# Optimization experiments

Measured on AMD Instinct MI355X. Metric: run time of the kernel, lower is better.

## Reference

```python
import jax, jax.numpy as jnp
import numpy as np

D_MODEL = 1024
NUM_HEADS = 16
D_K = D_MODEL // NUM_HEADS
D_FF = 4096
EPS = 1e-5


def _layer_norm(x, g, b):
    mu = jnp.mean(x, axis=-1, keepdims=True)
    var = jnp.mean(jnp.square(x - mu), axis=-1, keepdims=True)
    return (x - mu) * jax.lax.rsqrt(var + EPS) * g + b


def setup_inputs() -> dict:
    key = jax.random.key(0)
    ks = jax.random.split(key, 16)
    s = 0.02
    inp = {
        "x": jax.random.normal(ks[0], (2, 2048, D_MODEL), dtype=jnp.float32),
        # attention projections, torch Linear convention: W [out, in]
        "wq": jax.random.normal(ks[1], (D_MODEL, D_MODEL), dtype=jnp.float32) * s,
        "bq": jnp.zeros((D_MODEL,), jnp.float32),
        "wk": jax.random.normal(ks[2], (D_MODEL, D_MODEL), dtype=jnp.float32) * s,
        "bk": jnp.zeros((D_MODEL,), jnp.float32),
        "wv": jax.random.normal(ks[3], (D_MODEL, D_MODEL), dtype=jnp.float32) * s,
        "bv": jnp.zeros((D_MODEL,), jnp.float32),
        "wo": jax.random.normal(ks[4], (D_MODEL, D_MODEL), dtype=jnp.float32) * s,
        "bo": jnp.zeros((D_MODEL,), jnp.float32),
        "ln1_g": jnp.ones((D_MODEL,), jnp.float32),
        "ln1_b": jnp.zeros((D_MODEL,), jnp.float32),
        "w1": jax.random.normal(ks[5], (D_FF, D_MODEL), dtype=jnp.float32) * s,
        "b1": jnp.zeros((D_FF,), jnp.float32),
        "w2": jax.random.normal(ks[6], (D_MODEL, D_FF), dtype=jnp.float32) * s,
        "b2": jnp.zeros((D_MODEL,), jnp.float32),
        "ln2_g": jnp.ones((D_MODEL,), jnp.float32),
        "ln2_b": jnp.zeros((D_MODEL,), jnp.float32),
    }
    return inp


def reference(x, wq, bq, wk, bk, wv, bv, wo, bo, ln1_g, ln1_b,
              w1, b1, w2, b2, ln2_g, ln2_b):
    B, S, D = x.shape
    H, Dk = NUM_HEADS, D_K
    # projections -> [B, H, S, Dk]
    q = (x @ wq.T + bq).reshape(B, S, H, Dk).transpose(0, 2, 1, 3)
    k = (x @ wk.T + bk).reshape(B, S, H, Dk).transpose(0, 2, 1, 3)
    v = (x @ wv.T + bv).reshape(B, S, H, Dk).transpose(0, 2, 1, 3)
    # explicit [B,H,S,S] scores (faithful to source, memory-bound)
    scores = jnp.einsum("bhqd,bhkd->bhqk", q, k) / jnp.sqrt(jnp.float32(Dk))
    attn = jax.nn.softmax(scores, axis=-1)
    ctx = jnp.einsum("bhqk,bhkd->bhqd", attn, v)
    ctx = ctx.transpose(0, 2, 1, 3).reshape(B, S, D)
    attn_out = _layer_norm(ctx @ wo.T + bo + x, ln1_g, ln1_b)
    # feed-forward (post-LN residual), GELU (erf, torch default)
    h = jax.nn.gelu(attn_out @ w1.T + b1, approximate=False)
    ff = h @ w2.T + b2
    return _layer_norm(ff + attn_out, ln2_g, ln2_b)
```

## Files before the change

### kernel.cpp

```cpp
#include <hip/hip_runtime.h>
#include <math.h>

#define DM   1024
#define SL   2048
#define NB   2
#define NH   16
#define DKH  64
#define DFF  4096
#define NTOK 4096

typedef unsigned short u16;
typedef unsigned int u32;
typedef __attribute__((ext_vector_type(8))) short bf16x8;
typedef __attribute__((ext_vector_type(4))) float f32x4;
typedef __attribute__((ext_vector_type(16))) float f32x16;

typedef __attribute__((address_space(1))) void gvoid;
typedef __attribute__((address_space(3))) void lvoid;

#define QSCALE 0.18033688011112042f

__device__ __forceinline__ u16 f2bf(float f) {
  union { float f; unsigned u; } v; v.f = f;
  unsigned r = (v.u + 0x7fffu + ((v.u >> 16) & 1u)) >> 16;
  return (u16)r;
}
__device__ __forceinline__ float bf2f(u16 h) {
  union { unsigned u; float f; } v; v.u = ((unsigned)h) << 16; return v.f;
}
__device__ __forceinline__ void gld16(const u16* g, u16* l) {
  __builtin_amdgcn_global_load_lds((gvoid*)g, (lvoid*)l, 16, 0, 0);
}

__global__ __launch_bounds__(256)
void cvt_all(const float* __restrict__ x,  const float* __restrict__ wq,
             const float* __restrict__ wk, const float* __restrict__ wv,
             const float* __restrict__ wo, const float* __restrict__ w1,
             const float* __restrict__ w2,
             u16* __restrict__ xb, u16* __restrict__ wqb, u16* __restrict__ wkb,
             u16* __restrict__ wvb, u16* __restrict__ wob, u16* __restrict__ w1b,
             u16* __restrict__ w2b) {
  const int total = 4194304;
  for (int i = blockIdx.x * blockDim.x + threadIdx.x; i < total;
       i += gridDim.x * blockDim.x) {
    const float* src; u16* dst; int off;
    if      (i < 1048576) { src = x;  dst = xb;  off = i; }
    else if (i < 1310720) { src = wq; dst = wqb; off = i - 1048576; }
    else if (i < 1572864) { src = wk; dst = wkb; off = i - 1310720; }
    else if (i < 1835008) { src = wv; dst = wvb; off = i - 1572864; }
    else if (i < 2097152) { src = wo; dst = wob; off = i - 1835008; }
    else if (i < 3145728) { src = w1; dst = w1b; off = i - 2097152; }
    else                  { src = w2; dst = w2b; off = i - 3145728; }
    float4 v = ((const float4*)src)[off];
    ushort4 o = { f2bf(v.x), f2bf(v.y), f2bf(v.z), f2bf(v.w) };
    ((ushort4*)dst)[off] = o;
  }
}

#define BM 128
#define BN 128
#define BK 64

template <int EPI>
__global__ __launch_bounds__(256, 2)
void gemm_bt(const u16* __restrict__ A, const u16* __restrict__ W,
             const float* __restrict__ bias, const float* __restrict__ residf,
             const u16* __restrict__ residb, void* __restrict__ out,
             int M, int N, int K) {
  __shared__ u16 smem[2][2][BM * BK];
  const int tid = threadIdx.x;
  const int lane = tid & 63;
  const int wid  = tid >> 6;
  const int r16  = lane & 15;
  const int hi   = lane >> 4;
  const int wm = wid >> 1, wn = wid & 1;
  const int bm = blockIdx.x * BM;
  const int bn = blockIdx.y * BN;

  const int srow  = tid >> 3;
  const int sslot = (tid & 7) ^ (srow & 7);
  const size_t aoff = (size_t)(bm + srow) * K + sslot * 8;
  const size_t boff = (size_t)(bn + srow) * K + sslot * 8;

  f32x4 acc[4][4] = {};
  const int nk = K / BK;
  int cur = 0;

  auto STAGE = [&](int buf, int kt) {
    const u16* ga = A + aoff + kt * BK;
    const u16* gb = W + boff + kt * BK;
    u16* la = &smem[buf][0][wid * 512];
    u16* lb = &smem[buf][1][wid * 512];
#pragma unroll
    for (int i = 0; i < 4; ++i) {
      gld16(ga + (size_t)i * 32 * K, la + i * 2048);
      gld16(gb + (size_t)i * 32 * K, lb + i * 2048);
    }
  };

  STAGE(0, 0);
  __syncthreads();

  for (int kt = 0; kt < nk; ++kt) {
    if (kt + 1 < nk) STAGE(cur ^ 1, kt + 1);
    const u16* la = &smem[cur][0][0];
    const u16* lb = &smem[cur][1][0];
#pragma unroll
    for (int kk = 0; kk < 2; ++kk) {
      const int swz = ((kk * 4 + hi) ^ (r16 & 7)) * 8;
      bf16x8 af[4], bfr[4];
#pragma unroll
      for (int i = 0; i < 4; ++i)
        af[i] = *(const bf16x8*)&la[(wm * 64 + i * 16 + r16) * 64 + swz];
#pragma unroll
      for (int j = 0; j < 4; ++j)
        bfr[j] = *(const bf16x8*)&lb[(wn * 64 + j * 16 + r16) * 64 + swz];
      __builtin_amdgcn_s_setprio(1);
#pragma unroll
      for (int i = 0; i < 4; ++i)
#pragma unroll
        for (int j = 0; j < 4; ++j)
          acc[i][j] = __builtin_amdgcn_mfma_f32_16x16x32_bf16(af[i], bfr[j],
                                                              acc[i][j], 0, 0, 0);
      __builtin_amdgcn_s_setprio(0);
    }
    __syncthreads();
    cur ^= 1;
  }

#pragma unroll
  for (int i = 0; i < 4; ++i) {
#pragma unroll
    for (int j = 0; j < 4; ++j) {
      const int c  = bn + wn * 64 + j * 16 + r16;
      const int r0 = bm + wm * 64 + i * 16 + hi * 4;
      const float bv = bias[c];
#pragma unroll
      for (int rr = 0; rr < 4; ++rr) {
        const int r = r0 + rr;
        float v = acc[i][j][rr] + bv;
        if (EPI == 3) {
          ((float*)out)[(size_t)r * N + c] = v + residf[(size_t)r * N + c];
        } else if (EPI == 4) {
          const float gl = 0.5f * v * (1.0f + erff(v * 0.7071067811865475f));
          ((u16*)out)[(size_t)r * N + c] = f2bf(gl);
        } else {
          ((float*)out)[(size_t)r * N + c] = v + bf2f(residb[(size_t)r * N + c]);
        }
      }
    }
  }
}

__global__ __launch_bounds__(256, 2)
void gemm_qkv(const u16* __restrict__ A, const u16* __restrict__ wq,
              const u16* __restrict__ wk, const u16* __restrict__ wv,
              const float* __restrict__ bq, const float* __restrict__ bk,
              const float* __restrict__ bv,
              u16* __restrict__ qo, u16* __restrict__ ko, u16* __restrict__ vo) {
  __shared__ u16 smem[2][2][BM * BK];
  const int tid = threadIdx.x;
  const int lane = tid & 63;
  const int wid  = tid >> 6;
  const int r16  = lane & 15;
  const int hi   = lane >> 4;
  const int wm = wid >> 1, wn = wid & 1;
  const int bm = blockIdx.x * BM;
  const int sel = blockIdx.y >> 3;
  const int bn  = (blockIdx.y & 7) * BN;
  const u16* W = sel == 0 ? wq : sel == 1 ? wk : wv;
  const float* bias = sel == 0 ? bq : sel == 1 ? bk : bv;
  const int K = DM, N = DM;

  const int srow  = tid >> 3;
  const int sslot = (tid & 7) ^ (srow & 7);
  const size_t aoff = (size_t)(bm + srow) * K + sslot * 8;
  const size_t boff = (size_t)(bn + srow) * K + sslot * 8;

  f32x4 acc[4][4] = {};
  int cur = 0;

  auto STAGE = [&](int buf, int kt) {
    const u16* ga = A + aoff + kt * BK;
    const u16* gb = W + boff + kt * BK;
    u16* la = &smem[buf][0][wid * 512];
    u16* lb = &smem[buf][1][wid * 512];
#pragma unroll
    for (int i = 0; i < 4; ++i) {
      gld16(ga + (size_t)i * 32 * K, la + i * 2048);
      gld16(gb + (size_t)i * 32 * K, lb + i * 2048);
    }
  };

  STAGE(0, 0);
  __syncthreads();

  for (int kt = 0; kt < 16; ++kt) {
    if (kt + 1 < 16) STAGE(cur ^ 1, kt + 1);
    const u16* la = &smem[cur][0][0];
    const u16* lb = &smem[cur][1][0];
#pragma unroll
    for (int kk = 0; kk < 2; ++kk) {
      const int swz = ((kk * 4 + hi) ^ (r16 & 7)) * 8;
      bf16x8 af[4], bfr[4];
#pragma unroll
      for (int i = 0; i < 4; ++i)
        af[i] = *(const bf16x8*)&la[(wm * 64 + i * 16 + r16) * 64 + swz];
#pragma unroll
      for (int j = 0; j < 4; ++j)
        bfr[j] = *(const bf16x8*)&lb[(wn * 64 + j * 16 + r16) * 64 + swz];
      __builtin_amdgcn_s_setprio(1);
#pragma unroll
      for (int i = 0; i < 4; ++i)
#pragma unroll
        for (int j = 0; j < 4; ++j)
          acc[i][j] = __builtin_amdgcn_mfma_f32_16x16x32_bf16(af[i], bfr[j],
                                                              acc[i][j], 0, 0, 0);
      __builtin_amdgcn_s_setprio(0);
    }
    __syncthreads();
    cur ^= 1;
  }

#pragma unroll
  for (int i = 0; i < 4; ++i) {
#pragma unroll
    for (int j = 0; j < 4; ++j) {
      const int c  = bn + wn * 64 + j * 16 + r16;
      const int r0 = bm + wm * 64 + i * 16 + hi * 4;
      const float bvv = bias[c];
#pragma unroll
      for (int rr = 0; rr < 4; ++rr) {
        const int r = r0 + rr;
        const float v = acc[i][j][rr] + bvv;
        if (sel == 0) {
          qo[(size_t)r * N + c] = f2bf(v * QSCALE);
        } else if (sel == 1) {
          ko[(size_t)r * N + c] = f2bf(v);
        } else {
          const int b = r >> 11, s = r & 2047;
          const int hh = c >> 6, dk = c & 63;
          vo[((size_t)((b * NH + hh) * DKH + dk)) * SL + s] = f2bf(v);
        }
      }
    }
  }
}

__global__ __launch_bounds__(256, 2)
void attn(const u16* __restrict__ q, const u16* __restrict__ k,
          const u16* __restrict__ vt, u16* __restrict__ ctx) {
  __shared__ u16 kl[2][64 * 64];
  __shared__ u16 vl[2][64 * 64];

  const int tid = threadIdx.x;
  const int lane = tid & 63, wid = tid >> 6;
  const int l31 = lane & 31, h = lane >> 5;
  const int rs = l31 & 7;
  const int bh = blockIdx.x, b = bh >> 4, hh = bh & 15;
  const int qg = blockIdx.y * 128 + wid * 32 + l31;

  bf16x8 qf[4];
#pragma unroll
  for (int kq = 0; kq < 4; ++kq)
    qf[kq] = *(const bf16x8*)(q + (size_t)(b * SL + qg) * DM + hh * DKH +
                              kq * 16 + h * 8);

  f32x16 o0 = {}, o1 = {};
  float mrun = -1e30f, lrun = 0.f;

  const int srow  = tid >> 3;
  const int sslot = (tid & 7) ^ (srow & 7);

  auto STAGE = [&](int buf, int t) {
    const u16* gk = k + (size_t)(b * SL + t * 64 + srow) * DM + hh * DKH + sslot * 8;
    const u16* gv = vt + (size_t)(bh * DKH + srow) * SL + t * 64 + sslot * 8;
    u16* lk = &kl[buf][wid * 512];
    u16* lv = &vl[buf][wid * 512];
#pragma unroll
    for (int i = 0; i < 2; ++i) {
      gld16(gk + (size_t)i * 32 * DM, lk + i * 2048);
      gld16(gv + (size_t)i * 32 * SL, lv + i * 2048);
    }
  };

  auto TILE = [&](int buf) {
    const u16* lk = kl[buf];
    const u16* lv = vl[buf];
    f32x16 s0 = {}, s1 = {};
    __builtin_amdgcn_s_setprio(1);
#pragma unroll
    for (int kq = 0; kq < 4; ++kq) {
      const int ls = 2 * kq + h;
      bf16x8 k0 = *(const bf16x8*)&lk[l31 * 64 + ((ls ^ rs) * 8)];
      bf16x8 k1 = *(const bf16x8*)&lk[(l31 + 32) * 64 + ((ls ^ rs) * 8)];
      s0 = __builtin_amdgcn_mfma_f32_32x32x16_bf16(k0, qf[kq], s0, 0, 0, 0);
      s1 = __builtin_amdgcn_mfma_f32_32x32x16_bf16(k1, qf[kq], s1, 0, 0, 0);
    }
    __builtin_amdgcn_s_setprio(0);

    float mx = fmaxf(s0[0], s0[1]);
#pragma unroll
    for (int r = 2; r < 16; ++r) mx = fmaxf(mx, s0[r]);
#pragma unroll
    for (int r = 0; r < 16; ++r) mx = fmaxf(mx, s1[r]);
    {
      float ta = mx, tb = mx;
      asm volatile("v_permlane32_swap_b32 %0, %1" : "+v"(ta), "+v"(tb));
      mx = fmaxf(ta, tb);
    }
    if (!__all(mx <= mrun + 11.0f)) {
      const float mn = fmaxf(mrun, mx);
      const float al = __builtin_amdgcn_exp2f(mrun - mn);
      mrun = mn;
      lrun *= al;
      o0 *= al; o1 *= al;
    }
    float lsum = 0.f;
#pragma unroll
    for (int r = 0; r < 16; ++r) {
      s0[r] = __builtin_amdgcn_exp2f(s0[r] - mrun); lsum += s0[r];
    }
#pragma unroll
    for (int r = 0; r < 16; ++r) {
      s1[r] = __builtin_amdgcn_exp2f(s1[r] - mrun); lsum += s1[r];
    }
    lrun += lsum;

    u32 A[16];
#pragma unroll
    for (int r = 0; r < 8; ++r)
      asm("v_cvt_pk_bf16_f32 %0, %1, %2"
          : "=v"(A[r]) : "v"(s0[2 * r]), "v"(s0[2 * r + 1]));
#pragma unroll
    for (int r = 0; r < 8; ++r)
      asm("v_cvt_pk_bf16_f32 %0, %1, %2"
          : "=v"(A[8 + r]) : "v"(s1[2 * r]), "v"(s1[2 * r + 1]));
#pragma unroll
    for (int g = 0; g < 4; ++g) {
      asm volatile("v_permlane32_swap_b32 %0, %1" : "+v"(A[4 * g + 0]), "+v"(A[4 * g + 2]));
      asm volatile("v_permlane32_swap_b32 %0, %1" : "+v"(A[4 * g + 1]), "+v"(A[4 * g + 3]));
    }

    __builtin_amdgcn_s_setprio(1);
#pragma unroll
    for (int ks = 0; ks < 4; ++ks) {
      union { u32 u[4]; bf16x8 hv; } pb;
      pb.u[0] = A[4 * ks + 0]; pb.u[1] = A[4 * ks + 1];
      pb.u[2] = A[4 * ks + 2]; pb.u[3] = A[4 * ks + 3];
      const int ls = 2 * ks + h;
      bf16x8 v0 = *(const bf16x8*)&lv[l31 * 64 + ((ls ^ rs) * 8)];
      bf16x8 v1 = *(const bf16x8*)&lv[(l31 + 32) * 64 + ((ls ^ rs) * 8)];
      o0 = __builtin_amdgcn_mfma_f32_32x32x16_bf16(v0, pb.hv, o0, 0, 0, 0);
      o1 = __builtin_amdgcn_mfma_f32_32x32x16_bf16(v1, pb.hv, o1, 0, 0, 0);
    }
    __builtin_amdgcn_s_setprio(0);
  };

  STAGE(0, 0);
  __syncthreads();
  int cur = 0;
  for (int t = 0; t < SL / 64; ++t) {
    if (t + 1 < SL / 64) STAGE(cur ^ 1, t + 1);
    TILE(cur);
    __syncthreads();
    cur ^= 1;
  }

  float ta = lrun, tb = lrun;
  asm volatile("v_permlane32_swap_b32 %0, %1" : "+v"(ta), "+v"(tb));
  const float rl = 1.f / (ta + tb);
  const size_t obase = (size_t)(b * SL + qg) * DM + hh * DKH;
#pragma unroll
  for (int df = 0; df < 2; ++df) {
#pragma unroll
    for (int r2 = 0; r2 < 4; ++r2) {
      const int dk0 = 8 * r2 + 4 * h + 32 * df;
      ushort4 st;
      if (df == 0) {
        st.x = f2bf(o0[4 * r2 + 0] * rl); st.y = f2bf(o0[4 * r2 + 1] * rl);
        st.z = f2bf(o0[4 * r2 + 2] * rl); st.w = f2bf(o0[4 * r2 + 3] * rl);
      } else {
        st.x = f2bf(o1[4 * r2 + 0] * rl); st.y = f2bf(o1[4 * r2 + 1] * rl);
        st.z = f2bf(o1[4 * r2 + 2] * rl); st.w = f2bf(o1[4 * r2 + 3] * rl);
      }
      *(ushort4*)(ctx + obase + dk0) = st;
    }
  }
}

__global__ __launch_bounds__(256)
void ln_k(const float* __restrict__ in, const float* __restrict__ g,
          const float* __restrict__ be, float* __restrict__ outf,
          u16* __restrict__ outb) {
  const int row = blockIdx.x;
  const int tid = threadIdx.x;
  const float4 x4 = ((const float4*)(in + (size_t)row * DM))[tid];
  float s  = x4.x + x4.y + x4.z + x4.w;
  float s2 = x4.x * x4.x + x4.y * x4.y + x4.z * x4.z + x4.w * x4.w;
#pragma unroll
  for (int d = 1; d < 64; d <<= 1) {
    s  += __shfl_xor(s, d);
    s2 += __shfl_xor(s2, d);
  }
  __shared__ float ps[8];
  const int wid = tid >> 6, lane = tid & 63;
  if (lane == 0) { ps[wid] = s; ps[wid + 4] = s2; }
  __syncthreads();
  const float S  = ps[0] + ps[1] + ps[2] + ps[3];
  const float S2 = ps[4] + ps[5] + ps[6] + ps[7];
  const float mu = S * (1.f / DM);
  const float var = S2 * (1.f / DM) - mu * mu;
  const float rstd = 1.f / sqrtf(var + 1e-5f);
  const float4 gv = ((const float4*)g)[tid];
  const float4 bv = ((const float4*)be)[tid];
  float4 o;
  o.x = (x4.x - mu) * rstd * gv.x + bv.x;
  o.y = (x4.y - mu) * rstd * gv.y + bv.y;
  o.z = (x4.z - mu) * rstd * gv.z + bv.z;
  o.w = (x4.w - mu) * rstd * gv.w + bv.w;
  if (outf) ((float4*)(outf + (size_t)row * DM))[tid] = o;
  if (outb) {
    ushort4 ob = { f2bf(o.x), f2bf(o.y), f2bf(o.z), f2bf(o.w) };
    ((ushort4*)(outb + (size_t)row * DM))[tid] = ob;
  }
}

extern "C" void kernel_launch(void* const* d_in, const int* in_sizes, int n_in,
                              void* d_out, int out_size, void* d_ws, size_t ws_size,
                              hipStream_t stream) {
  const float* x   = (const float*)d_in[0];
  const float* wq  = (const float*)d_in[1];
  const float* bq  = (const float*)d_in[2];
  const float* wk  = (const float*)d_in[3];
  const float* bk  = (const float*)d_in[4];
  const float* wv  = (const float*)d_in[5];
  const float* bv  = (const float*)d_in[6];
  const float* wo  = (const float*)d_in[7];
  const float* bo  = (const float*)d_in[8];
  const float* g1  = (const float*)d_in[9];
  const float* be1 = (const float*)d_in[10];
  const float* w1  = (const float*)d_in[11];
  const float* b1  = (const float*)d_in[12];
  const float* w2  = (const float*)d_in[13];
  const float* b2  = (const float*)d_in[14];
  const float* g2  = (const float*)d_in[15];
  const float* be2 = (const float*)d_in[16];

  if (ws_size < ((size_t)80 << 20)) return;

  char* ws = (char*)d_ws;
  u16*  xb   = (u16*)(ws);
  u16*  wqb  = (u16*)(ws + ((size_t)8  << 20));
  u16*  wkb  = (u16*)(ws + ((size_t)10 << 20));
  u16*  wvb  = (u16*)(ws + ((size_t)12 << 20));
  u16*  wob  = (u16*)(ws + ((size_t)14 << 20));
  u16*  w1b  = (u16*)(ws + ((size_t)16 << 20));
  u16*  w2b  = (u16*)(ws + ((size_t)24 << 20));
  u16*  qbuf = (u16*)(ws + ((size_t)32 << 20));
  u16*  kbuf = (u16*)(ws + ((size_t)40 << 20));
  u16*  vtb  = (u16*)(ws + ((size_t)48 << 20));
  u16*  ctx  = (u16*)(ws + ((size_t)56 << 20));
  float* ores = (float*)(ws + ((size_t)64 << 20));
  u16*  aob  = xb;
  u16*  hb   = qbuf;
  float* ff  = ores;

  float* out = (float*)d_out;
  dim3 blk(256);

  cvt_all<<<2048, blk, 0, stream>>>(x, wq, wk, wv, wo, w1, w2,
                                    xb, wqb, wkb, wvb, wob, w1b, w2b);
  gemm_qkv<<<dim3(32, 24), blk, 0, stream>>>(xb, wqb, wkb, wvb, bq, bk, bv,
                                             qbuf, kbuf, vtb);
  attn<<<dim3(32, 16), blk, 0, stream>>>(qbuf, kbuf, vtb, ctx);
  gemm_bt<3><<<dim3(32, 8), blk, 0, stream>>>(ctx, wob, bo, x, nullptr, ores, NTOK, DM, DM);
  ln_k<<<4096, blk, 0, stream>>>(ores, g1, be1, nullptr, aob);
  gemm_bt<4><<<dim3(32, 32), blk, 0, stream>>>(aob, w1b, b1, nullptr, nullptr, hb, NTOK, DFF, DM);
  gemm_bt<5><<<dim3(32, 8), blk, 0, stream>>>(hb, w2b, b2, nullptr, aob, ff, NTOK, DM, DFF);
  ln_k<<<4096, blk, 0, stream>>>(ff, g2, be2, out, nullptr);
}
```

Measured before the change: 235.0 us.

## Use 256x256-tile 8-wave GEMM with phased pipelining for QKV and FFN1

Adds a new gemm256 kernel with 256x256 output tiles, 512 threads (8 waves), half-tile staged double buffering, and interleaved LDS loads, MFMA bursts and barriers. It also remaps block IDs to group tiles for L2 locality. It replaces the 128x128 QKV GEMM and the GELU FFN1 GEMM, aiming to raise per-block data reuse and hide global-load latency. The cost is many more registers per thread (32 accumulator vectors), fewer blocks (192/256 on a large-CU device), and a more fragile hand-tuned sync schedule.

```diff
diff --git a/kernel.cpp b/kernel.cpp
--- a/kernel.cpp
+++ b/kernel.cpp
@@ -57,6 +57,146 @@
   }
 }
 
+template <int MODE>
+__global__ __launch_bounds__(512, 2)
+void gemm256(const u16* __restrict__ A, const u16* __restrict__ Wq,
+             const u16* __restrict__ Wk, const u16* __restrict__ Wv,
+             const float* __restrict__ Bq, const float* __restrict__ Bk,
+             const float* __restrict__ Bv,
+             u16* __restrict__ qo, u16* __restrict__ ko, u16* __restrict__ vo,
+             int K) {
+  __shared__ u16 lds[2][2][2][128 * 64];
+
+  const int tid  = threadIdx.x;
+  const int lane = tid & 63;
+  const int wid  = tid >> 6;
+  const int r16  = lane & 15;
+  const int hi   = lane >> 4;
+  const int wr   = wid >> 2;
+  const int wc   = wid & 3;
+  const int nkt  = K >> 6;
+
+  const int lid = blockIdx.y * 16 + blockIdx.x;
+  const int nwg = (MODE == 0) ? 192 : 256;
+  const int cpx = nwg >> 3;
+  const int l2  = (lid & 7) * cpx + (lid >> 3);
+  const int bx2 = l2 & 15, by2 = l2 >> 4;
+
+  const int bm  = bx2 * 256;
+  int sel = 0, bnl;
+  const u16* W; const float* bias;
+  if (MODE == 0) {
+    sel = by2 >> 2;  bnl = (by2 & 3) * 256;
+    W = sel == 0 ? Wq : sel == 1 ? Wk : Wv;
+    bias = sel == 0 ? Bq : sel == 1 ? Bk : Bv;
+  } else {
+    bnl = by2 * 256; W = Wq; bias = Bq;
+  }
+
+  const int strow = tid >> 3;
+  const int stslt = tid & 7;
+  const int ssrc  = stslt ^ (strow & 7);
+
+  auto STAGEH = [&](int kt, int op, int hf) {
+    const u16* src = (op == 0) ? A : W;
+    const int  gb  = (op == 0) ? bm : bnl;
+    const u16* g = src + (size_t)(gb + hf * 128 + strow) * K + kt * 64 + ssrc * 8;
+    u16* d = &lds[kt & 1][op][hf][tid * 8];
+    gld16(g, d);
+    gld16(g + (size_t)64 * K, d + 4096);
+  };
+
+  f32x4 acc[8][4] = {};
+
+  STAGEH(0, 1, 0); STAGEH(0, 1, 1); STAGEH(0, 0, 0); STAGEH(0, 0, 1);
+  STAGEH(1, 1, 0); STAGEH(1, 1, 1);
+  asm volatile("s_waitcnt vmcnt(4)" ::: "memory");
+  __builtin_amdgcn_s_barrier();
+
+#define GPHASE(PH, SKT, SOP, SHF, VMTAIL)                                     \
+  {                                                                           \
+    bf16x8 af[2][2];                                                          \
+    _Pragma("unroll")                                                         \
+    for (int mm = 0; mm < 2; ++mm)                                            \
+      _Pragma("unroll")                                                       \
+      for (int kk = 0; kk < 2; ++kk) {                                        \
+        const int row = ((PH) * 2 + mm) * 16 + r16;                           \
+        af[mm][kk] = *(const bf16x8*)&la[row * 64 +                           \
+                        (((kk * 4 + hi) ^ (r16 & 7)) * 8)];                   \
+      }                                                                       \
+    if ((PH) == 0) {                                                          \
+      _Pragma("unroll")                                                       \
+      for (int n = 0; n < 4; ++n)                                             \
+        _Pragma("unroll")                                                     \
+        for (int kk = 0; kk < 2; ++kk) {                                      \
+          const int row = brow0 + n * 16 + r16;                               \
+          bfr[n][kk] = *(const bf16x8*)&lbh[row * 64 +                        \
+                          (((kk * 4 + hi) ^ (r16 & 7)) * 8)];                 \
+        }                                                                     \
+    }                                                                         \
+    if ((SKT) < nkt) STAGEH((SKT), (SOP), (SHF));                             \
+    __builtin_amdgcn_s_barrier();                                             \
+    asm volatile("s_waitcnt lgkmcnt(0)" ::: "memory");                        \
+    __builtin_amdgcn_sched_barrier(0);                                        \
+    __builtin_amdgcn_s_setprio(1);                                            \
+    _Pragma("unroll")                                                         \
+    for (int mm = 0; mm < 2; ++mm)                                            \
+      _Pragma("unroll")                                                       \
+      for (int n = 0; n < 4; ++n)                                             \
+        _Pragma("unroll")                                                     \
+        for (int kk = 0; kk < 2; ++kk)                                        \
+          acc[(PH) * 2 + mm][n] = __builtin_amdgcn_mfma_f32_16x16x32_bf16(    \
+              af[mm][kk], bfr[n][kk], acc[(PH) * 2 + mm][n], 0, 0, 0);        \
+    __builtin_amdgcn_s_setprio(0);                                            \
+    if ((VMTAIL) == 1) {                                                      \
+      if (T < nkt - 2) { asm volatile("s_waitcnt vmcnt(4)" ::: "memory"); }   \
+      else             { asm volatile("s_waitcnt vmcnt(0)" ::: "memory"); }   \
+    }                                                                         \
+    __builtin_amdgcn_s_barrier();                                             \
+  }
+
+  for (int T = 0; T < nkt; ++T) {
+    const u16* la  = lds[T & 1][0][wr];
+    const u16* lbh = lds[T & 1][1][wc >> 1];
+    const int brow0 = (wc & 1) * 64;
+    bf16x8 bfr[4][2];
+    GPHASE(0, T + 1, 0, 0, 0)
+    GPHASE(1, T + 1, 0, 1, 0)
+    GPHASE(2, T + 2, 1, 0, 0)
+    GPHASE(3, T + 2, 1, 1, 1)
+  }
+#undef GPHASE
+
+#pragma unroll
+  for (int m = 0; m < 8; ++m) {
+#pragma unroll
+    for (int n = 0; n < 4; ++n) {
+      const int cg  = bnl + wc * 64 + n * 16 + r16;
+      const int rg0 = bm + wr * 128 + m * 16 + hi * 4;
+      const float bv = bias[cg];
+#pragma unroll
+      for (int rr = 0; rr < 4; ++rr) {
+        const int rg = rg0 + rr;
+        const float v = acc[m][n][rr] + bv;
+        if (MODE == 0) {
+          if (sel == 0) {
+            qo[(size_t)rg * DM + cg] = f2bf(v * QSCALE);
+          } else if (sel == 1) {
+            ko[(size_t)rg * DM + cg] = f2bf(v);
+          } else {
+            const int b = rg >> 11, s = rg & 2047;
+            const int hh = cg >> 6, dk = cg & 63;
+            vo[((size_t)((b * NH + hh) * DKH + dk)) * SL + s] = f2bf(v);
+          }
+        } else {
+          const float gl = 0.5f * v * (1.0f + erff(v * 0.7071067811865475f));
+          qo[(size_t)rg * DFF + cg] = f2bf(gl);
+        }
+      }
+    }
+  }
+}
+
 #define BM 128
 #define BN 128
 #define BK 64
@@ -141,106 +281,8 @@
         float v = acc[i][j][rr] + bv;
         if (EPI == 3) {
           ((float*)out)[(size_t)r * N + c] = v + residf[(size_t)r * N + c];
-        } else if (EPI == 4) {
-          const float gl = 0.5f * v * (1.0f + erff(v * 0.7071067811865475f));
-          ((u16*)out)[(size_t)r * N + c] = f2bf(gl);
         } else {
           ((float*)out)[(size_t)r * N + c] = v + bf2f(residb[(size_t)r * N + c]);
-        }
-      }
-    }
-  }
-}
-
-__global__ __launch_bounds__(256, 2)
-void gemm_qkv(const u16* __restrict__ A, const u16* __restrict__ wq,
-              const u16* __restrict__ wk, const u16* __restrict__ wv,
-              const float* __restrict__ bq, const float* __restrict__ bk,
-              const float* __restrict__ bv,
-              u16* __restrict__ qo, u16* __restrict__ ko, u16* __restrict__ vo) {
-  __shared__ u16 smem[2][2][BM * BK];
-  const int tid = threadIdx.x;
-  const int lane = tid & 63;
-  const int wid  = tid >> 6;
-  const int r16  = lane & 15;
-  const int hi   = lane >> 4;
-  const int wm = wid >> 1, wn = wid & 1;
-  const int bm = blockIdx.x * BM;
-  const int sel = blockIdx.y >> 3;
-  const int bn  = (blockIdx.y & 7) * BN;
-  const u16* W = sel == 0 ? wq : sel == 1 ? wk : wv;
-  const float* bias = sel == 0 ? bq : sel == 1 ? bk : bv;
-  const int K = DM, N = DM;
-
-  const int srow  = tid >> 3;
-  const int sslot = (tid & 7) ^ (srow & 7);
-  const size_t aoff = (size_t)(bm + srow) * K + sslot * 8;
-  const size_t boff = (size_t)(bn + srow) * K + sslot * 8;
-
-  f32x4 acc[4][4] = {};
-  int cur = 0;
-
-  auto STAGE = [&](int buf, int kt) {
-    const u16* ga = A + aoff + kt * BK;
-    const u16* gb = W + boff + kt * BK;
-    u16* la = &smem[buf][0][wid * 512];
-    u16* lb = &smem[buf][1][wid * 512];
-#pragma unroll
-    for (int i = 0; i < 4; ++i) {
-      gld16(ga + (size_t)i * 32 * K, la + i * 2048);
-      gld16(gb + (size_t)i * 32 * K, lb + i * 2048);
-    }
-  };
-
-  STAGE(0, 0);
-  __syncthreads();
-
-  for (int kt = 0; kt < 16; ++kt) {
-    if (kt + 1 < 16) STAGE(cur ^ 1, kt + 1);
-    const u16* la = &smem[cur][0][0];
-    const u16* lb = &smem[cur][1][0];
-#pragma unroll
-    for (int kk = 0; kk < 2; ++kk) {
-      const int swz = ((kk * 4 + hi) ^ (r16 & 7)) * 8;
-      bf16x8 af[4], bfr[4];
-#pragma unroll
-      for (int i = 0; i < 4; ++i)
-        af[i] = *(const bf16x8*)&la[(wm * 64 + i * 16 + r16) * 64 + swz];
-#pragma unroll
-      for (int j = 0; j < 4; ++j)
-        bfr[j] = *(const bf16x8*)&lb[(wn * 64 + j * 16 + r16) * 64 + swz];
-      __builtin_amdgcn_s_setprio(1);
-#pragma unroll
-      for (int i = 0; i < 4; ++i)
-#pragma unroll
-        for (int j = 0; j < 4; ++j)
-          acc[i][j] = __builtin_amdgcn_mfma_f32_16x16x32_bf16(af[i], bfr[j],
-                                                              acc[i][j], 0, 0, 0);
-      __builtin_amdgcn_s_setprio(0);
-    }
-    __syncthreads();
-    cur ^= 1;
-  }
-
-#pragma unroll
-  for (int i = 0; i < 4; ++i) {
-#pragma unroll
-    for (int j = 0; j < 4; ++j) {
-      const int c  = bn + wn * 64 + j * 16 + r16;
-      const int r0 = bm + wm * 64 + i * 16 + hi * 4;
-      const float bvv = bias[c];
-#pragma unroll
-      for (int rr = 0; rr < 4; ++rr) {
-        const int r = r0 + rr;
-        const float v = acc[i][j][rr] + bvv;
-        if (sel == 0) {
-          qo[(size_t)r * N + c] = f2bf(v * QSCALE);
-        } else if (sel == 1) {
-          ko[(size_t)r * N + c] = f2bf(v);
-        } else {
-          const int b = r >> 11, s = r & 2047;
-          const int hh = c >> 6, dk = c & 63;
-          vo[((size_t)((b * NH + hh) * DKH + dk)) * SL + s] = f2bf(v);
         }
       }
     }
@@ -471,12 +513,14 @@
 
   cvt_all<<<2048, blk, 0, stream>>>(x, wq, wk, wv, wo, w1, w2,
                                     xb, wqb, wkb, wvb, wob, w1b, w2b);
-  gemm_qkv<<<dim3(32, 24), blk, 0, stream>>>(xb, wqb, wkb, wvb, bq, bk, bv,
-                                             qbuf, kbuf, vtb);
+  gemm256<0><<<dim3(16, 12), 512, 0, stream>>>(xb, wqb, wkb, wvb, bq, bk, bv,
+                                               qbuf, kbuf, vtb, DM);
   attn<<<dim3(32, 16), blk, 0, stream>>>(qbuf, kbuf, vtb, ctx);
   gemm_bt<3><<<dim3(32, 8), blk, 0, stream>>>(ctx, wob, bo, x, nullptr, ores, NTOK, DM, DM);
   ln_k<<<4096, blk, 0, stream>>>(ores, g1, be1, nullptr, aob);
-  gemm_bt<4><<<dim3(32, 32), blk, 0, stream>>>(aob, w1b, b1, nullptr, nullptr, hb, NTOK, DFF, DM);
+  gemm256<1><<<dim3(16, 16), 512, 0, stream>>>(aob, w1b, nullptr, nullptr,
+                                               b1, nullptr, nullptr,
+                                               hb, nullptr, nullptr, DM);
   gemm_bt<5><<<dim3(32, 8), blk, 0, stream>>>(hb, w2b, b2, nullptr, aob, ff, NTOK, DM, DFF);
   ln_k<<<4096, blk, 0, stream>>>(ff, g2, be2, out, nullptr);
 }
```

New measurement: 247.7 us. 1.05x slower.

## Remap workgroups across XCDs and store pre-LayerNorm residual sums in bf16

Applied to the files above, without the earlier changes.

Workgroup IDs in the GEMMs and the attention kernel are permuted so that consecutive tiles sharing A rows or the same head land on the same XCD (a stride-8 round-robin remap), aiming for better L2 reuse on the chiplet layout. The pre-LayerNorm residual outputs of the output-projection and FFN2 GEMMs are now stored as bf16 instead of fp32, and the LayerNorm kernel is templated to read bf16 input. This halves the bytes written and read between those GEMMs and LayerNorm, at the cost of rounding the residual sum to bf16 before normalisation.

```diff
diff --git a/kernel.cpp b/kernel.cpp
--- a/kernel.cpp
+++ b/kernel.cpp
@@ -74,8 +74,12 @@
   const int r16  = lane & 15;
   const int hi   = lane >> 4;
   const int wm = wid >> 1, wn = wid & 1;
-  const int bm = blockIdx.x * BM;
-  const int bn = blockIdx.y * BN;
+
+  const int nwg = gridDim.x * gridDim.y;
+  const int lid = blockIdx.y * 32 + blockIdx.x;
+  const int l2  = (lid & 7) * (nwg >> 3) + (lid >> 3);
+  const int bm  = (l2 & 31) * BM;
+  const int bn  = (l2 >> 5) * BN;
 
   const int srow  = tid >> 3;
   const int sslot = (tid & 7) ^ (srow & 7);
@@ -140,12 +144,13 @@
         const int r = r0 + rr;
         float v = acc[i][j][rr] + bv;
         if (EPI == 3) {
-          ((float*)out)[(size_t)r * N + c] = v + residf[(size_t)r * N + c];
+          ((u16*)out)[(size_t)r * N + c] = f2bf(v + residf[(size_t)r * N + c]);
         } else if (EPI == 4) {
           const float gl = 0.5f * v * (1.0f + erff(v * 0.7071067811865475f));
           ((u16*)out)[(size_t)r * N + c] = f2bf(gl);
         } else {
-          ((float*)out)[(size_t)r * N + c] = v + bf2f(residb[(size_t)r * N + c]);
+          ((u16*)out)[(size_t)r * N + c] =
+              f2bf(v + bf2f(residb[(size_t)r * N + c]));
         }
       }
     }
@@ -165,9 +170,13 @@
   const int r16  = lane & 15;
   const int hi   = lane >> 4;
   const int wm = wid >> 1, wn = wid & 1;
-  const int bm = blockIdx.x * BM;
-  const int sel = blockIdx.y >> 3;
-  const int bn  = (blockIdx.y & 7) * BN;
+
+  const int lid = blockIdx.y * 32 + blockIdx.x;
+  const int l2  = (lid & 7) * 96 + (lid >> 3);
+  const int bm  = (l2 & 31) * BM;
+  const int by  = l2 >> 5;
+  const int sel = by >> 3;
+  const int bn  = (by & 7) * BN;
   const u16* W = sel == 0 ? wq : sel == 1 ? wk : wv;
   const float* bias = sel == 0 ? bq : sel == 1 ? bk : bv;
   const int K = DM, N = DM;
@@ -257,8 +266,13 @@
   const int lane = tid & 63, wid = tid >> 6;
   const int l31 = lane & 31, h = lane >> 5;
   const int rs = l31 & 7;
-  const int bh = blockIdx.x, b = bh >> 4, hh = bh & 15;
-  const int qg = blockIdx.y * 128 + wid * 32 + l31;
+
+  const int lid = blockIdx.y * 32 + blockIdx.x;
+  const int rr_ = lid & 31;
+  const int bh = (rr_ & 7) * 4 + (rr_ >> 3);
+  const int qb = lid >> 5;
+  const int b = bh >> 4, hh = bh & 15;
+  const int qg = qb * 128 + wid * 32 + l31;
 
   bf16x8 qf[4];
 #pragma unroll
@@ -389,13 +403,20 @@
   }
 }
 
+template <int INBF>
 __global__ __launch_bounds__(256)
-void ln_k(const float* __restrict__ in, const float* __restrict__ g,
+void ln_k(const void* __restrict__ inp, const float* __restrict__ g,
           const float* __restrict__ be, float* __restrict__ outf,
           u16* __restrict__ outb) {
   const int row = blockIdx.x;
   const int tid = threadIdx.x;
-  const float4 x4 = ((const float4*)(in + (size_t)row * DM))[tid];
+  float4 x4;
+  if (INBF) {
+    ushort4 h4 = ((const ushort4*)((const u16*)inp + (size_t)row * DM))[tid];
+    x4.x = bf2f(h4.x); x4.y = bf2f(h4.y); x4.z = bf2f(h4.z); x4.w = bf2f(h4.w);
+  } else {
+    x4 = ((const float4*)((const float*)inp + (size_t)row * DM))[tid];
+  }
   float s  = x4.x + x4.y + x4.z + x4.w;
   float s2 = x4.x * x4.x + x4.y * x4.y + x4.z * x4.z + x4.w * x4.w;
 #pragma unroll
@@ -461,10 +482,10 @@
   u16*  kbuf = (u16*)(ws + ((size_t)40 << 20));
   u16*  vtb  = (u16*)(ws + ((size_t)48 << 20));
   u16*  ctx  = (u16*)(ws + ((size_t)56 << 20));
-  float* ores = (float*)(ws + ((size_t)64 << 20));
+  u16*  oresb = (u16*)(ws + ((size_t)64 << 20));
+  u16*  ffb   = (u16*)(ws + ((size_t)72 << 20));
   u16*  aob  = xb;
   u16*  hb   = qbuf;
-  float* ff  = ores;
 
   float* out = (float*)d_out;
   dim3 blk(256);
@@ -474,9 +495,12 @@
   gemm_qkv<<<dim3(32, 24), blk, 0, stream>>>(xb, wqb, wkb, wvb, bq, bk, bv,
                                              qbuf, kbuf, vtb);
   attn<<<dim3(32, 16), blk, 0, stream>>>(qbuf, kbuf, vtb, ctx);
-  gemm_bt<3><<<dim3(32, 8), blk, 0, stream>>>(ctx, wob, bo, x, nullptr, ores, NTOK, DM, DM);
-  ln_k<<<4096, blk, 0, stream>>>(ores, g1, be1, nullptr, aob);
-  gemm_bt<4><<<dim3(32, 32), blk, 0, stream>>>(aob, w1b, b1, nullptr, nullptr, hb, NTOK, DFF, DM);
-  gemm_bt<5><<<dim3(32, 8), blk, 0, stream>>>(hb, w2b, b2, nullptr, aob, ff, NTOK, DM, DFF);
-  ln_k<<<4096, blk, 0, stream>>>(ff, g2, be2, out, nullptr);
-}
+  gemm_bt<3><<<dim3(32, 8), blk, 0, stream>>>(ctx, wob, bo, x, nullptr, oresb,
+                                              NTOK, DM, DM);
+  ln_k<1><<<4096, blk, 0, stream>>>(oresb, g1, be1, nullptr, aob);
+  gemm_bt<4><<<dim3(32, 32), blk, 0, stream>>>(aob, w1b, b1, nullptr, nullptr,
+                                               hb, NTOK, DFF, DM);
+  gemm_bt<5><<<dim3(32, 8), blk, 0, stream>>>(hb, w2b, b2, nullptr, aob, ffb,
+                                              NTOK, DM, DFF);
+  ln_k<1><<<4096, blk, 0, stream>>>(ffb, g2, be2, out, nullptr);
+}
```

Result: slower. 250.4 us (+6.6%).
